# Kernel tuning notes

Hardware: AMD Instinct MI355X
Metric: run time of the kernel (lower is better)

The kernel has to match this reference:

```python
import jax, jax.numpy as jnp
import numpy as np

T, B, D, ATTN_D, K = 128, 2048, 1024, 1024, 8


def setup_inputs() -> dict:
    key = jax.random.key(0)
    k1, k2, k3, k4 = jax.random.split(key, 4)
    h_context = jax.random.normal(k1, (T, B, D), dtype=jnp.float32)
    offsets = jax.random.randint(k2, (B,), 0, T, dtype=jnp.int32)
    stc_lens = jnp.full((B,), T, dtype=jnp.int32)
    # one separator per sample at position T: segment [0, T], identical math to no-sep case
    sep_lst = jnp.full((B, 1), T, dtype=jnp.int32)
    # xavier-normal-ish init for the attention MLP weights (torch Linear layout: [out, in])
    W1 = jax.random.normal(k3, (ATTN_D, D), dtype=jnp.float32) * np.sqrt(2.0 / (D + ATTN_D))
    W2 = jax.random.normal(k4, (1, ATTN_D), dtype=jnp.float32) * np.sqrt(2.0 / (ATTN_D + 1))
    return {"h_context": h_context, "offsets": offsets, "stc_lens": stc_lens,
            "sep_lst": sep_lst, "no_local": 0, "W1": W1, "W2": W2}


def reference(h_context, offsets, stc_lens, sep_lst, no_local, W1, W2):
    # h_context: [T, B, D] (seq-first). no_local is unused (as in the original forward).
    Kw = 8
    Tn, Bn, Dn = h_context.shape
    L = 2 * Kw  # max window length: range(pos-K, pos+K) has at most 2K elements

    # Segment bounds: with a single separator per sample, pos is either in
    # segment [0, sep] or in segment [sep+1, stc_len] (mirrors the loop in forward).
    sep = sep_lst[:, 0]
    in_seg1 = offsets <= sep
    start = jnp.where(in_seg1, jnp.maximum(offsets - Kw, 0), jnp.maximum(offsets - Kw, sep + 1))
    end = jnp.where(in_seg1, jnp.minimum(offsets + Kw, sep), jnp.minimum(offsets + Kw, stc_lens))

    idx = start[:, None] + jnp.arange(L, dtype=start.dtype)  # [B, L]
    valid = idx < end[:, None]                               # [B, L] True = real token
    idx_c = jnp.clip(idx, 0, Tn - 1)

    # Irregular per-sample gather: blk[b, l] = h_context[idx[b, l], b]
    blk = h_context[idx_c, jnp.arange(Bn)[:, None]]          # [B, L, D]
    blk = jnp.where(valid[..., None], blk, jnp.zeros((), blk.dtype))  # zero padding (= F.pad)

    blk_t = blk.transpose(1, 0, 2)                           # [L, B, D] (matches h_context_blk)
    # attn_trans: Linear(D->attn_d) -> tanh -> Linear(attn_d->1) -> Softmax(dim=1)
    a = jnp.tanh(jnp.einsum('lbd,ad->lba', blk_t, W1))       # [L, B, attn_d]
    s = jnp.einsum('lba,oa->lbo', a, W2)                     # [L, B, 1]
    s = jax.nn.softmax(s, axis=1)                            # softmax over batch dim (dim=1)
    score = jnp.mean(s, axis=2)                              # [L, B]

    # masked softmax over the window dim (dim=0); padded rows -> -inf
    score = jnp.where(valid.T, score, -jnp.inf)
    score = jax.nn.softmax(score, axis=0)                    # [L, B]

    # bmm: [B,1,L] @ [B,L,D] -> [B,1,D]
    h_blank = jnp.einsum('lb,bld->bd', score, blk)[:, None, :]
    return h_blank
```

## Files before the change

kernel.cpp:

```cpp
#include <hip/hip_runtime.h>

#define T_DIM 128
#define B_DIM 2048
#define D_DIM 1024
#define KW 8
#define NCOL (B_DIM * 16)

#define PL   2064
#define BUFB (8 * PL)

typedef _Float16 f16x8 __attribute__((ext_vector_type(8)));
typedef _Float16 f16x4 __attribute__((ext_vector_type(4)));
typedef float    f32x16 __attribute__((ext_vector_type(16)));

static __device__ __forceinline__ int imax(int a, int b) { return a > b ? a : b; }
static __device__ __forceinline__ int imin(int a, int b) { return a < b ? a : b; }

__global__ void k_cvt_w1(const float* __restrict__ W1, _Float16* __restrict__ W1f) {
    int i  = blockIdx.x * 256 + threadIdx.x;
    int m  = i >> 6;
    int kc = i & 63;
    const float* src = W1 + (size_t)m * D_DIM + kc * 16;
    float4 x0 = *(const float4*)(src);
    float4 x1 = *(const float4*)(src + 4);
    float4 x2 = *(const float4*)(src + 8);
    float4 x3 = *(const float4*)(src + 12);
    f16x8 h0, h1;
    h0[0] = (_Float16)x0.x; h0[1] = (_Float16)x0.y;
    h0[2] = (_Float16)x0.z; h0[3] = (_Float16)x0.w;
    h0[4] = (_Float16)x1.x; h0[5] = (_Float16)x1.y;
    h0[6] = (_Float16)x1.z; h0[7] = (_Float16)x1.w;
    h1[0] = (_Float16)x2.x; h1[1] = (_Float16)x2.y;
    h1[2] = (_Float16)x2.z; h1[3] = (_Float16)x2.w;
    h1[4] = (_Float16)x3.x; h1[5] = (_Float16)x3.y;
    h1[6] = (_Float16)x3.z; h1[7] = (_Float16)x3.w;
    _Float16* dst = W1f + ((size_t)kc * 1024 + m) * 16;
    *(f16x8*)(dst)     = h0;
    *(f16x8*)(dst + 8) = h1;
}

__launch_bounds__(512, 2)
__global__ void k_gemm(const float* __restrict__ hctx,
                       const int*   __restrict__ offsets,
                       const int*   __restrict__ stc,
                       const int*   __restrict__ sep_l,
                       const _Float16* __restrict__ W1f,
                       const float* __restrict__ W2,
                       float* __restrict__ s_raw) {
    __shared__ __align__(16) char ldsx[2 * BUFB];
    __shared__ float red[8][64];

    int cg   = blockIdx.x;
    int tid  = threadIdx.x;
    int wid  = tid >> 6;
    int lane = tid & 63;
    int lr   = lane & 31;
    int hi   = lane >> 5;

    const float* sbase[4];
    int svalid[4];
    int wr_off[4];
#pragma unroll
    for (int rr = 0; rr < 4; ++rr) {
        int colL = wid * 8 + rr * 2 + hi;
        int col  = cg * 64 + colL;
        int b    = col >> 4;
        int li   = col & 15;
        int off = offsets[b];
        int sep = sep_l[b];
        int st  = stc[b];
        bool in1 = (off <= sep);
        int start = in1 ? imax(off - KW, 0)   : imax(off - KW, sep + 1);
        int end   = in1 ? imin(off + KW, sep) : imin(off + KW, st);
        int idx = start + li;
        svalid[rr] = (idx < end) ? 1 : 0;
        int tc = imin(imax(idx, 0), T_DIM - 1);
        sbase[rr] = hctx + ((size_t)tc * B_DIM + b) * D_DIM + lr * 4;
        wr_off[rr] = (lr >> 2) * PL + ((lr >> 1) & 1) * 1024 + colL * 16 + (lr & 1) * 8;
    }

    const _Float16* ap = W1f + (size_t)(wid * 128 + lr) * 16 + hi * 8;
    int rd_off = hi * 1024 + lr * 16;

    f32x16 acc[4][2];
#pragma unroll
    for (int f = 0; f < 4; ++f)
#pragma unroll
        for (int nf = 0; nf < 2; ++nf)
#pragma unroll
            for (int i = 0; i < 16; ++i) acc[f][nf][i] = 0.f;

    {
        float4 z = {0.f, 0.f, 0.f, 0.f};
#pragma unroll
        for (int rr = 0; rr < 4; ++rr) {
            float4 x = svalid[rr] ? *(const float4*)(sbase[rr]) : z;
            f16x4 h;
            h[0] = (_Float16)x.x; h[1] = (_Float16)x.y;
            h[2] = (_Float16)x.z; h[3] = (_Float16)x.w;
            *(f16x4*)(ldsx + wr_off[rr]) = h;
        }
    }

    f16x8 a0[4], a1[4];
#pragma unroll
    for (int f = 0; f < 4; ++f) a0[f] = *(const f16x8*)(ap + f * 512);
#pragma unroll
    for (int f = 0; f < 4; ++f) a1[f] = *(const f16x8*)(ap + 16384 + f * 512);

    __syncthreads();

    f16x8 b0[2];
    {
        const char* bp = ldsx + rd_off;
        b0[0] = *(const f16x8*)(bp);
        b0[1] = *(const f16x8*)(bp + 512);
    }

    for (int c = 0; c < 8; ++c) {
        int bufr = (c & 1) * BUFB;

        float4 xn[4];
        if (c < 7) {
            int k0 = (c + 1) * 128;
            float4 z = {0.f, 0.f, 0.f, 0.f};
#pragma unroll
            for (int rr = 0; rr < 4; ++rr)
                xn[rr] = svalid[rr] ? *(const float4*)(sbase[rr] + k0) : z;
        }

#pragma unroll
        for (int kcL = 0; kcL < 8; ++kcL) {
            int kc = c * 8 + kcL;
            int ka = (kc + 2) & 63;

            f16x8 a2[4];
#pragma unroll
            for (int f = 0; f < 4; ++f)
                a2[f] = *(const f16x8*)(ap + (size_t)ka * 16384 + f * 512);

            f16x8 b1[2];
            if (kcL < 7) {
                const char* bp = ldsx + bufr + (kcL + 1) * PL + rd_off;
                b1[0] = *(const f16x8*)(bp);
                b1[1] = *(const f16x8*)(bp + 512);
            }

#pragma unroll
            for (int f = 0; f < 4; ++f)
                acc[f][0] = __builtin_amdgcn_mfma_f32_32x32x16_f16(
                    a0[f], b0[0], acc[f][0], 0, 0, 0);
#pragma unroll
            for (int f = 0; f < 4; ++f)
                acc[f][1] = __builtin_amdgcn_mfma_f32_32x32x16_f16(
                    a0[f], b0[1], acc[f][1], 0, 0, 0);

#pragma unroll
            for (int f = 0; f < 4; ++f) { a0[f] = a1[f]; a1[f] = a2[f]; }
            if (kcL < 7) { b0[0] = b1[0]; b0[1] = b1[1]; }
        }

        if (c < 7) {
            int bufw = ((c + 1) & 1) * BUFB;
#pragma unroll
            for (int rr = 0; rr < 4; ++rr) {
                f16x4 h;
                h[0] = (_Float16)xn[rr].x; h[1] = (_Float16)xn[rr].y;
                h[2] = (_Float16)xn[rr].z; h[3] = (_Float16)xn[rr].w;
                *(f16x4*)(ldsx + bufw + wr_off[rr]) = h;
            }
        }
        __syncthreads();
        if (c < 7) {
            const char* bp = ldsx + ((c + 1) & 1) * BUFB + rd_off;
            b0[0] = *(const f16x8*)(bp);
            b0[1] = *(const f16x8*)(bp + 512);
        }
    }

    int m_wg = wid * 128;
    float sp0 = 0.f, sp1 = 0.f;
#pragma unroll
    for (int f = 0; f < 4; ++f) {
#pragma unroll
        for (int rg = 0; rg < 4; ++rg) {
            int mbase = m_wg + f * 32 + rg * 8 + hi * 4;
            float4 w2v = *(const float4*)(W2 + mbase);
            float w2a[4] = {w2v.x, w2v.y, w2v.z, w2v.w};
#pragma unroll
            for (int j = 0; j < 4; ++j) {
                float w2 = w2a[j];
                {
                    float x = acc[f][0][rg * 4 + j];
                    float e = __expf(2.f * x);
                    sp0 += w2 * (1.f - 2.f / (e + 1.f));
                }
                {
                    float x = acc[f][1][rg * 4 + j];
                    float e = __expf(2.f * x);
                    sp1 += w2 * (1.f - 2.f / (e + 1.f));
                }
            }
        }
    }
    sp0 += __shfl_xor(sp0, 32, 64);
    sp1 += __shfl_xor(sp1, 32, 64);

    if (hi == 0) {
        red[wid][lr]      = sp0;
        red[wid][32 + lr] = sp1;
    }
    __syncthreads();
    if (tid < 64) {
        float s = 0.f;
#pragma unroll
        for (int w = 0; w < 8; ++w) s += red[w][tid];
        s_raw[cg * 64 + tid] = s;
    }
}

__global__ void k_smax1(const float* __restrict__ s_raw,
                        float* __restrict__ lstats ) {
    int l = blockIdx.x;
    int t = threadIdx.x;
    int lane = t & 63, wid = t >> 6;

    float v[8];
    float mx = -__builtin_inff();
#pragma unroll
    for (int i = 0; i < 8; ++i) {
        int b = i * 256 + t;
        float x = s_raw[b * 16 + l];
        v[i] = x;
        mx = fmaxf(mx, x);
    }
#pragma unroll
    for (int d = 1; d < 64; d <<= 1) mx = fmaxf(mx, __shfl_xor(mx, d, 64));
    __shared__ float rm[4];
    if (lane == 0) rm[wid] = mx;
    __syncthreads();
    mx = fmaxf(fmaxf(rm[0], rm[1]), fmaxf(rm[2], rm[3]));

    float se = 0.f;
#pragma unroll
    for (int i = 0; i < 8; ++i) se += __expf(v[i] - mx);
#pragma unroll
    for (int d = 1; d < 64; d <<= 1) se += __shfl_xor(se, d, 64);
    __shared__ float rs[4];
    if (lane == 0) rs[wid] = se;
    __syncthreads();
    if (t == 0) {
        lstats[l]      = mx;
        lstats[16 + l] = rs[0] + rs[1] + rs[2] + rs[3];
    }
}

__global__ void k_out(const float* __restrict__ hctx,
                      const int*   __restrict__ offsets,
                      const int*   __restrict__ stc,
                      const int*   __restrict__ sep_l,
                      const float* __restrict__ s_raw,
                      const float* __restrict__ lstats,
                      float* __restrict__ out) {
    int b = blockIdx.x;
    int t = threadIdx.x;

    int off = offsets[b];
    int sep = sep_l[b];
    int st  = stc[b];
    bool in1 = (off <= sep);
    int start = in1 ? imax(off - KW, 0)   : imax(off - KW, sep + 1);
    int end   = in1 ? imin(off + KW, sep) : imin(off + KW, st);

    float p[16];
    float m2 = -__builtin_inff();
#pragma unroll
    for (int l = 0; l < 16; ++l) {
        bool valid = (start + l) < end;
        float s = s_raw[b * 16 + l];
        float pl = __expf(s - lstats[l]) / lstats[16 + l];
        p[l] = valid ? pl : -__builtin_inff();
        m2 = fmaxf(m2, p[l]);
    }
    float q[16];
    float qs = 0.f;
#pragma unroll
    for (int l = 0; l < 16; ++l) {
        float e = __expf(p[l] - m2);
        q[l] = e;
        qs += e;
    }
    float rqs = 1.f / qs;

    float4 acc = {0.f, 0.f, 0.f, 0.f};
#pragma unroll
    for (int l = 0; l < 16; ++l) {
        float wl = q[l] * rqs;
        if (wl > 0.f) {
            int tr = imin(imax(start + l, 0), T_DIM - 1);
            float4 x = *((const float4*)(hctx + ((size_t)tr * B_DIM + b) * D_DIM) + t);
            acc.x += wl * x.x; acc.y += wl * x.y;
            acc.z += wl * x.z; acc.w += wl * x.w;
        }
    }
    *((float4*)(out + (size_t)b * D_DIM) + t) = acc;
}

extern "C" void kernel_launch(void* const* d_in, const int* in_sizes, int n_in,
                              void* d_out, int out_size, void* d_ws, size_t ws_size,
                              hipStream_t stream) {
    const float* hctx    = (const float*)d_in[0];
    const int*   offsets = (const int*)d_in[1];
    const int*   stc     = (const int*)d_in[2];
    const int*   sep     = (const int*)d_in[3];
    const float* W1      = (const float*)d_in[5];
    const float* W2      = (const float*)d_in[6];
    float* out = (float*)d_out;

    char* ws = (char*)d_ws;
    _Float16* W1f    = (_Float16*)ws;
    float*    s_raw  = (float*)(ws + (2u << 20));
    float*    lstats = (float*)(ws + (2u << 20) + (128u << 10));

    hipLaunchKernelGGL(k_cvt_w1, dim3(256),  dim3(256), 0, stream, W1, W1f);
    hipLaunchKernelGGL(k_gemm,   dim3(512),  dim3(512), 0, stream,
                       hctx, offsets, stc, sep, W1f, W2, s_raw);
    hipLaunchKernelGGL(k_smax1,  dim3(16),   dim3(256), 0, stream, s_raw, lstats);
    hipLaunchKernelGGL(k_out,    dim3(2048), dim3(256), 0, stream,
                       hctx, offsets, stc, sep, s_raw, lstats, out);
}
```

Before: 136.8 us.

## Split GEMM attention dimension across two workgroups with partial score reduction

Each GEMM workgroup now covers half of the 1024 attention outputs using 256 threads instead of all 1024 with 512 threads. The grid doubles to 1024 blocks, and the two partial score sums are added in the softmax kernel, which also writes s_raw. The activation staging is reorganized so each thread loads 16 contiguous floats per chunk and writes one 16-byte fp16 vector. This aims to improve occupancy and wave distribution across CUs, at the cost of reading each activation tile twice (once per half) and an extra partial buffer.

```diff
diff --git a/kernel.cpp b/kernel.cpp
--- a/kernel.cpp
+++ b/kernel.cpp
@@ -7,14 +7,23 @@
 #define NCOL (B_DIM * 16)
 
 #define PL   2064
-#define BUFB (8 * PL)
+#define BUFB (4 * PL)
+#define CHUNKS 16
 
 typedef _Float16 f16x8 __attribute__((ext_vector_type(8)));
-typedef _Float16 f16x4 __attribute__((ext_vector_type(4)));
 typedef float    f32x16 __attribute__((ext_vector_type(16)));
 
 static __device__ __forceinline__ int imax(int a, int b) { return a > b ? a : b; }
 static __device__ __forceinline__ int imin(int a, int b) { return a < b ? a : b; }
+
+__device__ __forceinline__ f16x8 cvt2(float4 u, float4 v) {
+    f16x8 h;
+    h[0] = (_Float16)u.x; h[1] = (_Float16)u.y;
+    h[2] = (_Float16)u.z; h[3] = (_Float16)u.w;
+    h[4] = (_Float16)v.x; h[5] = (_Float16)v.y;
+    h[6] = (_Float16)v.z; h[7] = (_Float16)v.w;
+    return h;
+}
 
 __global__ void k_cvt_w1(const float* __restrict__ W1, _Float16* __restrict__ W1f) {
     int i  = blockIdx.x * 256 + threadIdx.x;
@@ -25,61 +34,49 @@
     float4 x1 = *(const float4*)(src + 4);
     float4 x2 = *(const float4*)(src + 8);
     float4 x3 = *(const float4*)(src + 12);
-    f16x8 h0, h1;
-    h0[0] = (_Float16)x0.x; h0[1] = (_Float16)x0.y;
-    h0[2] = (_Float16)x0.z; h0[3] = (_Float16)x0.w;
-    h0[4] = (_Float16)x1.x; h0[5] = (_Float16)x1.y;
-    h0[6] = (_Float16)x1.z; h0[7] = (_Float16)x1.w;
-    h1[0] = (_Float16)x2.x; h1[1] = (_Float16)x2.y;
-    h1[2] = (_Float16)x2.z; h1[3] = (_Float16)x2.w;
-    h1[4] = (_Float16)x3.x; h1[5] = (_Float16)x3.y;
-    h1[6] = (_Float16)x3.z; h1[7] = (_Float16)x3.w;
     _Float16* dst = W1f + ((size_t)kc * 1024 + m) * 16;
-    *(f16x8*)(dst)     = h0;
-    *(f16x8*)(dst + 8) = h1;
-}
-
-__launch_bounds__(512, 2)
+    *(f16x8*)(dst)     = cvt2(x0, x1);
+    *(f16x8*)(dst + 8) = cvt2(x2, x3);
+}
+
+__launch_bounds__(256, 2)
 __global__ void k_gemm(const float* __restrict__ hctx,
                        const int*   __restrict__ offsets,
                        const int*   __restrict__ stc,
                        const int*   __restrict__ sep_l,
                        const _Float16* __restrict__ W1f,
                        const float* __restrict__ W2,
-                       float* __restrict__ s_raw) {
+                       float* __restrict__ s_part ) {
     __shared__ __align__(16) char ldsx[2 * BUFB];
-    __shared__ float red[8][64];
-
-    int cg   = blockIdx.x;
+    __shared__ float red[4][64];
+
+    int bid  = blockIdx.x;
+    int mt   = bid & 1;
+    int cg   = bid >> 1;
     int tid  = threadIdx.x;
     int wid  = tid >> 6;
     int lane = tid & 63;
     int lr   = lane & 31;
     int hi   = lane >> 5;
 
-    const float* sbase[4];
-    int svalid[4];
-    int wr_off[4];
-#pragma unroll
-    for (int rr = 0; rr < 4; ++rr) {
-        int colL = wid * 8 + rr * 2 + hi;
-        int col  = cg * 64 + colL;
-        int b    = col >> 4;
-        int li   = col & 15;
-        int off = offsets[b];
-        int sep = sep_l[b];
-        int st  = stc[b];
-        bool in1 = (off <= sep);
-        int start = in1 ? imax(off - KW, 0)   : imax(off - KW, sep + 1);
-        int end   = in1 ? imin(off + KW, sep) : imin(off + KW, st);
-        int idx = start + li;
-        svalid[rr] = (idx < end) ? 1 : 0;
-        int tc = imin(imax(idx, 0), T_DIM - 1);
-        sbase[rr] = hctx + ((size_t)tc * B_DIM + b) * D_DIM + lr * 4;
-        wr_off[rr] = (lr >> 2) * PL + ((lr >> 1) & 1) * 1024 + colL * 16 + (lr & 1) * 8;
-    }
-
-    const _Float16* ap = W1f + (size_t)(wid * 128 + lr) * 16 + hi * 8;
+    int sc  = tid & 63;
+    int kcs = tid >> 6;
+    int col = cg * 64 + sc;
+    int b   = col >> 4;
+    int li  = col & 15;
+    int off = offsets[b];
+    int sep = sep_l[b];
+    int st  = stc[b];
+    bool in1 = (off <= sep);
+    int start = in1 ? imax(off - KW, 0)   : imax(off - KW, sep + 1);
+    int end   = in1 ? imin(off + KW, sep) : imin(off + KW, st);
+    int idx = start + li;
+    bool valid = (idx < end);
+    int tc = imin(imax(idx, 0), T_DIM - 1);
+    const float* sbase = hctx + ((size_t)tc * B_DIM + b) * D_DIM + kcs * 16;
+    int wr0 = kcs * PL + sc * 16;
+
+    const _Float16* ap = W1f + (size_t)(mt * 512 + wid * 128 + lr) * 16 + hi * 8;
     int rd_off = hi * 1024 + lr * 16;
 
     f32x16 acc[4][2];
@@ -90,16 +87,15 @@
 #pragma unroll
             for (int i = 0; i < 16; ++i) acc[f][nf][i] = 0.f;
 
+    float4 z = {0.f, 0.f, 0.f, 0.f};
+
     {
-        float4 z = {0.f, 0.f, 0.f, 0.f};
-#pragma unroll
-        for (int rr = 0; rr < 4; ++rr) {
-            float4 x = svalid[rr] ? *(const float4*)(sbase[rr]) : z;
-            f16x4 h;
-            h[0] = (_Float16)x.x; h[1] = (_Float16)x.y;
-            h[2] = (_Float16)x.z; h[3] = (_Float16)x.w;
-            *(f16x4*)(ldsx + wr_off[rr]) = h;
-        }
+        float4 x0 = valid ? *(const float4*)(sbase)      : z;
+        float4 x1 = valid ? *(const float4*)(sbase + 4)  : z;
+        float4 x2 = valid ? *(const float4*)(sbase + 8)  : z;
+        float4 x3 = valid ? *(const float4*)(sbase + 12) : z;
+        *(f16x8*)(ldsx + wr0)        = cvt2(x0, x1);
+        *(f16x8*)(ldsx + wr0 + 1024) = cvt2(x2, x3);
     }
 
     f16x8 a0[4], a1[4];
@@ -111,27 +107,24 @@
     __syncthreads();
 
     f16x8 b0[2];
-    {
-        const char* bp = ldsx + rd_off;
-        b0[0] = *(const f16x8*)(bp);
-        b0[1] = *(const f16x8*)(bp + 512);
-    }
-
-    for (int c = 0; c < 8; ++c) {
+    b0[0] = *(const f16x8*)(ldsx + rd_off);
+    b0[1] = *(const f16x8*)(ldsx + rd_off + 512);
+
+    for (int c = 0; c < CHUNKS; ++c) {
         int bufr = (c & 1) * BUFB;
 
-        float4 xn[4];
-        if (c < 7) {
-            int k0 = (c + 1) * 128;
-            float4 z = {0.f, 0.f, 0.f, 0.f};
-#pragma unroll
-            for (int rr = 0; rr < 4; ++rr)
-                xn[rr] = svalid[rr] ? *(const float4*)(sbase[rr] + k0) : z;
-        }
-
-#pragma unroll
-        for (int kcL = 0; kcL < 8; ++kcL) {
-            int kc = c * 8 + kcL;
+        float4 xn0, xn1, xn2, xn3;
+        if (c < CHUNKS - 1) {
+            const float* sp = sbase + (c + 1) * 64;
+            xn0 = valid ? *(const float4*)(sp)      : z;
+            xn1 = valid ? *(const float4*)(sp + 4)  : z;
+            xn2 = valid ? *(const float4*)(sp + 8)  : z;
+            xn3 = valid ? *(const float4*)(sp + 12) : z;
+        }
+
+#pragma unroll
+        for (int kcL = 0; kcL < 4; ++kcL) {
+            int kc = c * 4 + kcL;
             int ka = (kc + 2) & 63;
 
             f16x8 a2[4];
@@ -140,7 +133,7 @@
                 a2[f] = *(const f16x8*)(ap + (size_t)ka * 16384 + f * 512);
 
             f16x8 b1[2];
-            if (kcL < 7) {
+            if (kcL < 3) {
                 const char* bp = ldsx + bufr + (kcL + 1) * PL + rd_off;
                 b1[0] = *(const f16x8*)(bp);
                 b1[1] = *(const f16x8*)(bp + 512);
@@ -157,28 +150,23 @@
 
 #pragma unroll
             for (int f = 0; f < 4; ++f) { a0[f] = a1[f]; a1[f] = a2[f]; }
-            if (kcL < 7) { b0[0] = b1[0]; b0[1] = b1[1]; }
-        }
-
-        if (c < 7) {
+            if (kcL < 3) { b0[0] = b1[0]; b0[1] = b1[1]; }
+        }
+
+        if (c < CHUNKS - 1) {
             int bufw = ((c + 1) & 1) * BUFB;
-#pragma unroll
-            for (int rr = 0; rr < 4; ++rr) {
-                f16x4 h;
-                h[0] = (_Float16)xn[rr].x; h[1] = (_Float16)xn[rr].y;
-                h[2] = (_Float16)xn[rr].z; h[3] = (_Float16)xn[rr].w;
-                *(f16x4*)(ldsx + bufw + wr_off[rr]) = h;
-            }
+            *(f16x8*)(ldsx + bufw + wr0)        = cvt2(xn0, xn1);
+            *(f16x8*)(ldsx + bufw + wr0 + 1024) = cvt2(xn2, xn3);
         }
         __syncthreads();
-        if (c < 7) {
+        if (c < CHUNKS - 1) {
             const char* bp = ldsx + ((c + 1) & 1) * BUFB + rd_off;
             b0[0] = *(const f16x8*)(bp);
             b0[1] = *(const f16x8*)(bp + 512);
         }
     }
 
-    int m_wg = wid * 128;
+    int m_wg = mt * 512 + wid * 128;
     float sp0 = 0.f, sp1 = 0.f;
 #pragma unroll
     for (int f = 0; f < 4; ++f) {
@@ -212,14 +200,13 @@
     }
     __syncthreads();
     if (tid < 64) {
-        float s = 0.f;
-#pragma unroll
-        for (int w = 0; w < 8; ++w) s += red[w][tid];
-        s_raw[cg * 64 + tid] = s;
-    }
-}
-
-__global__ void k_smax1(const float* __restrict__ s_raw,
+        float s = red[0][tid] + red[1][tid] + red[2][tid] + red[3][tid];
+        s_part[(size_t)mt * NCOL + cg * 64 + tid] = s;
+    }
+}
+
+__global__ void k_smax1(const float* __restrict__ s_part,
+                        float* __restrict__ s_raw,
                         float* __restrict__ lstats ) {
     int l = blockIdx.x;
     int t = threadIdx.x;
@@ -230,8 +217,10 @@
 #pragma unroll
     for (int i = 0; i < 8; ++i) {
         int b = i * 256 + t;
-        float x = s_raw[b * 16 + l];
+        int id = b * 16 + l;
+        float x = s_part[id] + s_part[NCOL + id];
         v[i] = x;
+        s_raw[id] = x;
         mx = fmaxf(mx, x);
     }
 #pragma unroll
@@ -319,13 +308,15 @@
 
     char* ws = (char*)d_ws;
     _Float16* W1f    = (_Float16*)ws;
-    float*    s_raw  = (float*)(ws + (2u << 20));
-    float*    lstats = (float*)(ws + (2u << 20) + (128u << 10));
+    float*    s_part = (float*)(ws + (2u << 20));
+    float*    s_raw  = (float*)(ws + (2u << 20) + (256u << 10));
+    float*    lstats = (float*)(ws + (2u << 20) + (384u << 10));
 
     hipLaunchKernelGGL(k_cvt_w1, dim3(256),  dim3(256), 0, stream, W1, W1f);
-    hipLaunchKernelGGL(k_gemm,   dim3(512),  dim3(512), 0, stream,
-                       hctx, offsets, stc, sep, W1f, W2, s_raw);
-    hipLaunchKernelGGL(k_smax1,  dim3(16),   dim3(256), 0, stream, s_raw, lstats);
+    hipLaunchKernelGGL(k_gemm,   dim3(1024), dim3(256), 0, stream,
+                       hctx, offsets, stc, sep, W1f, W2, s_part);
+    hipLaunchKernelGGL(k_smax1,  dim3(16),   dim3(256), 0, stream,
+                       s_part, s_raw, lstats);
     hipLaunchKernelGGL(k_out,    dim3(2048), dim3(256), 0, stream,
                        hctx, offsets, stc, sep, s_raw, lstats, out);
 }
```

After: 217.2 us. 1.59x slower.
